# Optimization experiments

Hardware: AMD Instinct MI355X
Metric: run time of the kernel (lower is better)

Reference implementation:

```python
import jax, jax.numpy as jnp
import numpy as np

PATCH = 7
STRIDE = 1
ALPHA = 0.05


def extract_patches(im, p=PATCH, s=STRIDE):
    # im: (b, c, h, w) -> (b, n_patches, c*p*p)
    pat = jax.lax.conv_general_dilated_patches(im, (p, p), (s, s), 'VALID')  # (b, c*p*p, H', W')
    b, d = pat.shape[0], pat.shape[1]
    return pat.reshape(b, d, -1).transpose(0, 2, 1)


def _coherence_l2(xp, yp):
    # xp: (Ni, d) input patches, yp: (Nt, d) target patches, both fp16
    d = xp.shape[-1]
    x2 = jnp.sum(xp * xp, axis=-1)                     # (Ni,)
    y2 = jnp.sum(yp * yp, axis=-1)                     # (Nt,)
    cross = jnp.einsum('td,id->ti', yp, xp)            # (Nt, Ni)
    dist = (y2[:, None] + x2[None, :] - 2.0 * cross) / d
    # normalize each target row by its NN distance (+alpha), then min over targets
    dist = dist / (jnp.min(dist, axis=1, keepdims=True) + jnp.asarray(ALPHA, dist.dtype))
    return jnp.min(dist, axis=0).mean()


def setup_inputs() -> dict:
    key = jax.random.key(0)
    k1, k2 = jax.random.split(key)
    x = jax.random.normal(k1, (2, 3, 96, 96), dtype=jnp.float32)
    y = jax.random.normal(k2, (2, 3, 96, 96), dtype=jnp.float32)
    return {"x": x, "y": y}


def reference(x, y):
    x16 = x.astype(jnp.float16)
    y16 = y.astype(jnp.float16)
    xp = extract_patches(x16)   # (b, N, d)
    yp = extract_patches(y16)   # (b, N, d)
    per_image = jax.vmap(_coherence_l2)(xp, yp)  # (b,)
    return per_image.mean()
```

## Files before the change

kernel.cpp:

```cpp
#include <hip/hip_runtime.h>
#include <hip/hip_fp16.h>

#define IMGS 2
#define OW 90
#define NP 8100
#define HW 96
#define CH_STRIDE 9216
#define IMG_STRIDE 27648
#define KP 192
#define MP 8192
#define ALPHA 0.05f
#define INV_D (1.0f/147.0f)
#define PAD_SENTINEL 60000.0f

typedef _Float16 half8 __attribute__((ext_vector_type(8)));
typedef float floatx4 __attribute__((ext_vector_type(4)));

#define GLD_LDS16(gp, lp)                                                     \
    __builtin_amdgcn_global_load_lds(                                         \
        (const __attribute__((address_space(1))) void*)(gp),                  \
        (__attribute__((address_space(3))) void*)(lp), 16, 0, 0)

#define XP_OFF   0
#define YP_OFF   (XP_OFF + IMGS*MP*KP*2)
#define N2Y_OFF  (YP_OFF + IMGS*MP*KP*2)
#define RMIN_OFF (N2Y_OFF + IMGS*MP*4)
#define CMIN_OFF (RMIN_OFF + IMGS*MP*4)

__global__ __launch_bounds__(256) void k_build(const float* __restrict__ x,
                                               const float* __restrict__ y,
                                               char* __restrict__ wsb) {
    int tid = threadIdx.x;
    int hwv = tid >> 5;
    int l = tid & 31;
    int grow = blockIdx.x * 8 + hwv;
    int tensor = grow >> 14;
    int img = (grow >> 13) & 1;
    int row = grow & (MP - 1);
    const float* src = (tensor ? y : x) + img * IMG_STRIDE;
    int py = row / OW, px = row - py * OW;
    bool rvalid = row < NP;

    float vals[8];
#pragma unroll
    for (int j = 0; j < 8; j++) {
        int k = l * 8 + j;
        float v = 0.0f;
        if (rvalid && k < 147) {
            int c = k / 49;
            int rm = k - c * 49;
            int dy = rm / 7, dx = rm - dy * 7;
            v = src[c * CH_STRIDE + (py + dy) * HW + px + dx];
        }
        vals[j] = (float)(_Float16)v;
    }
    float ss16 = 0.0f;
#pragma unroll
    for (int j = 0; j < 8; j++) ss16 = fmaf(vals[j], vals[j], ss16);
#pragma unroll
    for (int m = 1; m < 32; m <<= 1) ss16 += __shfl_xor(ss16, m, 32);

    if (tensor && l == 0)
        ((float*)(wsb + N2Y_OFF))[img * MP + row] = rvalid ? ss16 : 0.0f;

    half8 h;
#pragma unroll
    for (int j = 0; j < 8; j++) {
        float f = vals[j];
        if (tensor) f *= -2.0f;
        h[j] = (_Float16)f;
    }
    if (l == 18) {
        h[3] = tensor ? (_Float16)1.0f
                      : (rvalid ? (_Float16)ss16 : (_Float16)PAD_SENTINEL);
        if (!tensor) h[4] = rvalid ? (_Float16)1.0f : (_Float16)0.0f;
    }
    if (l < 24) {
        _Float16* dst = (_Float16*)(wsb + (tensor ? YP_OFF : XP_OFF)) +
                        ((size_t)img * MP + row) * KP + l * 8;
        *(half8*)dst = h;
    }
    if (tid < 8) {
        int gi = blockIdx.x * 8 + tid;
        if (gi < IMGS * MP)
            ((int*)(wsb + RMIN_OFF))[gi] = 0x7f800000;
        else
            ((int*)(wsb + CMIN_OFF))[gi - IMGS * MP] = 0x7f800000;
    }
}

#define R2OFF 8192

#define STAGE64(mat, buf)                                                      \
    {                                                                          \
        int rb_ = w * 16;                                                      \
        _Pragma("unroll") for (int g_ = 0; g_ < 4; g_++) {                     \
            int r_ = rb_ + g_ * 4 + (lane >> 4);                               \
            int gc_ = (lane & 15) ^ (r_ & 7);                                  \
            GLD_LDS16((mat) + (size_t)r_ * KP + gc_ * 8,                       \
                      (buf) + (rb_ + g_ * 4) * 128);                           \
        }                                                                      \
        int r2_ = rb_ + (lane >> 2);                                           \
        int gc2_ = (lane & 3) ^ ((r2_ >> 1) & 3);                              \
        GLD_LDS16((mat) + (size_t)r2_ * KP + 128 + gc2_ * 8,                   \
                  (buf) + R2OFF + rb_ * 32);                                   \
    }

#define READFRAG(buf, row, ks)                                                 \
    ((ks) < 4 ? *(const half8*)(&(buf)[(row) * 128 +                           \
                                       ((((ks) * 4 + quad) ^ ((row) & 7)) * 8)]) \
              : *(const half8*)(&(buf)[R2OFF + (row) * 32 +                    \
                                       ((quad ^ (((row) >> 1) & 3)) * 8)]))

template <int PASS>
__global__ __launch_bounds__(256, 3) void k_gemm(char* __restrict__ wsb) {
    __shared__ __align__(16) _Float16 Buf[2][10240];
    int tid = threadIdx.x;
    int lane = tid & 63, w = tid >> 6;
    int quad = lane >> 4, col16 = lane & 15;
    int q = blockIdx.x;
    int rtile = blockIdx.y;
    int img = blockIdx.z;

    const _Float16* Res = (const _Float16*)(wsb + (PASS == 1 ? YP_OFF : XP_OFF)) +
                          ((size_t)img * MP + rtile * 128) * KP;
    const _Float16* Str = (const _Float16*)(wsb + (PASS == 1 ? XP_OFF : YP_OFF)) +
                          (size_t)img * MP * KP;

    STAGE64(Res, Buf[0]);
    STAGE64(Res + (size_t)64 * KP, Buf[1]);
    __syncthreads();
    half8 rf[4][5];
    const _Float16* rb = Buf[w >> 1];
#pragma unroll
    for (int i = 0; i < 4; i++)
#pragma unroll
        for (int c = 0; c < 5; c++)
            rf[i][c] = READFRAG(rb, i * 16 + col16, c);
    __syncthreads();
    STAGE64(Str + (size_t)(q * 16) * 64 * KP, Buf[0]);

    float rmin[4][4];
    float cmin[4];
#pragma unroll
    for (int i = 0; i < 4; i++) {
        cmin[i] = 1e30f;
#pragma unroll
        for (int j = 0; j < 4; j++) rmin[i][j] = 1e30f;
    }
    int s0 = (w & 1) * 32;

    for (int s = 0; s < 16; s++) {
        __syncthreads();
        if (s < 15)
            STAGE64(Str + (size_t)(q * 16 + s + 1) * 64 * KP, Buf[(s + 1) & 1]);
        const _Float16* sb = Buf[s & 1];
        floatx4 acc[8];
#pragma unroll
        for (int i = 0; i < 8; i++) acc[i] = (floatx4){0.f, 0.f, 0.f, 0.f};
#pragma unroll
        for (int ks = 0; ks < 5; ks++) {
            half8 sf0 = READFRAG(sb, s0 + col16, ks);
            half8 sf1 = READFRAG(sb, s0 + 16 + col16, ks);
            if (PASS == 1) {
#pragma unroll
                for (int i = 0; i < 4; i++) {
                    acc[i * 2] = __builtin_amdgcn_mfma_f32_16x16x32_f16(
                        rf[i][ks], sf0, acc[i * 2], 0, 0, 0);
                    acc[i * 2 + 1] = __builtin_amdgcn_mfma_f32_16x16x32_f16(
                        rf[i][ks], sf1, acc[i * 2 + 1], 0, 0, 0);
                }
            } else {
#pragma unroll
                for (int i = 0; i < 4; i++) {
                    acc[i] = __builtin_amdgcn_mfma_f32_16x16x32_f16(
                        sf0, rf[i][ks], acc[i], 0, 0, 0);
                    acc[4 + i] = __builtin_amdgcn_mfma_f32_16x16x32_f16(
                        sf1, rf[i][ks], acc[4 + i], 0, 0, 0);
                }
            }
        }
        if (PASS == 1) {
#pragma unroll
            for (int i = 0; i < 4; i++)
#pragma unroll
                for (int r = 0; r < 4; r++)
                    rmin[i][r] = fminf(rmin[i][r],
                                       fminf(acc[i * 2][r], acc[i * 2 + 1][r]));
        } else {
#pragma unroll
            for (int i = 0; i < 4; i++)
#pragma unroll
                for (int r = 0; r < 4; r++)
                    cmin[i] = fminf(cmin[i], fminf(acc[i][r], acc[4 + i][r]));
        }
    }

    if (PASS == 1) {
#pragma unroll
        for (int i = 0; i < 4; i++)
#pragma unroll
            for (int r = 0; r < 4; r++) {
                float best = rmin[i][r];
                best = fminf(best, __shfl_xor(best, 1, 16));
                best = fminf(best, __shfl_xor(best, 2, 16));
                best = fminf(best, __shfl_xor(best, 4, 16));
                best = fminf(best, __shfl_xor(best, 8, 16));
                int rg = rtile * 128 + (w >> 1) * 64 + i * 16 + quad * 4 + r;
                if (col16 == 0 && rg < NP)
                    atomicMin((int*)(wsb + RMIN_OFF) + img * MP + rg,
                              __float_as_int(best));
            }
    } else {
#pragma unroll
        for (int i = 0; i < 4; i++) {
            float best = cmin[i];
            best = fminf(best, __shfl_xor(best, 16, 64));
            best = fminf(best, __shfl_xor(best, 32, 64));
            int cg = rtile * 128 + (w >> 1) * 64 + i * 16 + col16;
            if (quad == 0)
                atomicMin((int*)(wsb + CMIN_OFF) + img * MP + cg,
                          __float_as_int(best));
        }
    }
}

__global__ __launch_bounds__(256) void k_rescale(char* __restrict__ wsb) {
    int gid = blockIdx.x * 256 + threadIdx.x;
    int chunk = gid % 24;
    int row = gid / 24;
    int r = row & (MP - 1);
    float rm = __int_as_float(((const int*)(wsb + RMIN_OFF))[row]);
    float y2 = ((const float*)(wsb + N2Y_OFF))[row];
    float d = (y2 + rm) * INV_D;
    float rp = INV_D / (d + ALPHA);
    _Float16* p = (_Float16*)(wsb + YP_OFF) + (size_t)row * KP + chunk * 8;
    half8 h = *(half8*)p;
#pragma unroll
    for (int j = 0; j < 8; j++) h[j] = (_Float16)((float)h[j] * rp);
    if (chunk == 18)
        h[4] = (r < NP) ? (_Float16)(rp * y2) : (_Float16)PAD_SENTINEL;
    *(half8*)p = h;
}

__global__ __launch_bounds__(256) void k_final(const char* __restrict__ wsb,
                                               float* __restrict__ out) {
    __shared__ float red[256];
    int tid = threadIdx.x;
    const int* cm = (const int*)(wsb + CMIN_OFF);
    float s = 0.0f;
    for (int i = tid; i < NP; i += 256) {
        s += __int_as_float(cm[i]);
        s += __int_as_float(cm[MP + i]);
    }
    red[tid] = s;
    __syncthreads();
    for (int st = 128; st > 0; st >>= 1) {
        if (tid < st) red[tid] += red[tid + st];
        __syncthreads();
    }
    if (tid == 0) out[0] = red[0] * (0.5f / NP);
}

extern "C" void kernel_launch(void* const* d_in, const int* in_sizes, int n_in,
                              void* d_out, int out_size, void* d_ws, size_t ws_size,
                              hipStream_t stream) {
    const float* x = (const float*)d_in[0];
    const float* y = (const float*)d_in[1];
    char* wsb = (char*)d_ws;
    float* out = (float*)d_out;

    k_build<<<4096, 256, 0, stream>>>(x, y, wsb);
    k_gemm<1><<<dim3(8, 64, IMGS), 256, 0, stream>>>(wsb);
    k_rescale<<<(IMGS * MP * 24) / 256, 256, 0, stream>>>(wsb);
    k_gemm<2><<<dim3(8, 64, IMGS), 256, 0, stream>>>(wsb);
    k_final<<<1, 256, 0, stream>>>(wsb, out);
}
```

Baseline: 167.2 us.

## Fuse row rescale into second GEMM pass and restructure MFMA tiling per wave

Drops the separate rescale kernel and the stored y-norm buffer. The y norm now sits in the augmented K column, so pass 1 yields the full row distance, and pass 2 scales each streamed target fragment on the fly by the reciprocal normalizer. Each wave now keeps all 128 resident rows in registers (8x5 fragments) and streams 16 target rows, so both passes share one min/atomic epilogue. This removes a kernel launch and a full read/write of the target patch matrix. In exchange it raises register pressure (occupancy hint lowered from 3 to 2) and adds per-step fp16 multiplies and global loads of row minima in pass 2.

```diff
diff --git a/kernel.cpp b/kernel.cpp
--- a/kernel.cpp
+++ b/kernel.cpp
@@ -23,8 +23,7 @@
 
 #define XP_OFF   0
 #define YP_OFF   (XP_OFF + IMGS*MP*KP*2)
-#define N2Y_OFF  (YP_OFF + IMGS*MP*KP*2)
-#define RMIN_OFF (N2Y_OFF + IMGS*MP*4)
+#define RMIN_OFF (YP_OFF + IMGS*MP*KP*2)
 #define CMIN_OFF (RMIN_OFF + IMGS*MP*4)
 
 __global__ __launch_bounds__(256) void k_build(const float* __restrict__ x,
@@ -60,9 +59,6 @@
 #pragma unroll
     for (int m = 1; m < 32; m <<= 1) ss16 += __shfl_xor(ss16, m, 32);
 
-    if (tensor && l == 0)
-        ((float*)(wsb + N2Y_OFF))[img * MP + row] = rvalid ? ss16 : 0.0f;
-
     half8 h;
 #pragma unroll
     for (int j = 0; j < 8; j++) {
@@ -71,9 +67,13 @@
         h[j] = (_Float16)f;
     }
     if (l == 18) {
-        h[3] = tensor ? (_Float16)1.0f
-                      : (rvalid ? (_Float16)ss16 : (_Float16)PAD_SENTINEL);
-        if (!tensor) h[4] = rvalid ? (_Float16)1.0f : (_Float16)0.0f;
+        if (tensor) {
+            h[3] = (_Float16)1.0f;
+            h[4] = rvalid ? (_Float16)ss16 : (_Float16)0.0f;
+        } else {
+            h[3] = rvalid ? (_Float16)ss16 : (_Float16)PAD_SENTINEL;
+            h[4] = rvalid ? (_Float16)1.0f : (_Float16)0.0f;
+        }
     }
     if (l < 24) {
         _Float16* dst = (_Float16*)(wsb + (tensor ? YP_OFF : XP_OFF)) +
@@ -113,7 +113,7 @@
                                        ((quad ^ (((row) >> 1) & 3)) * 8)]))
 
 template <int PASS>
-__global__ __launch_bounds__(256, 3) void k_gemm(char* __restrict__ wsb) {
+__global__ __launch_bounds__(256, 2) void k_gemm(char* __restrict__ wsb) {
     __shared__ __align__(16) _Float16 Buf[2][10240];
     int tid = threadIdx.x;
     int lane = tid & 63, w = tid >> 6;
@@ -130,117 +130,71 @@
     STAGE64(Res, Buf[0]);
     STAGE64(Res + (size_t)64 * KP, Buf[1]);
     __syncthreads();
-    half8 rf[4][5];
-    const _Float16* rb = Buf[w >> 1];
-#pragma unroll
-    for (int i = 0; i < 4; i++)
+    half8 rf[8][5];
+#pragma unroll
+    for (int i = 0; i < 8; i++) {
+        const _Float16* rb = (i < 4) ? Buf[0] : Buf[1];
 #pragma unroll
         for (int c = 0; c < 5; c++)
-            rf[i][c] = READFRAG(rb, i * 16 + col16, c);
+            rf[i][c] = READFRAG(rb, (i & 3) * 16 + col16, c);
+    }
     __syncthreads();
     STAGE64(Str + (size_t)(q * 16) * 64 * KP, Buf[0]);
 
-    float rmin[4][4];
-    float cmin[4];
-#pragma unroll
-    for (int i = 0; i < 4; i++) {
-        cmin[i] = 1e30f;
-#pragma unroll
-        for (int j = 0; j < 4; j++) rmin[i][j] = 1e30f;
-    }
-    int s0 = (w & 1) * 32;
+    float mn[8];
+#pragma unroll
+    for (int i = 0; i < 8; i++) mn[i] = 1e30f;
+    const int* RM = (const int*)(wsb + RMIN_OFF) + img * MP;
+    int srow = w * 16 + col16;
 
     for (int s = 0; s < 16; s++) {
         __syncthreads();
         if (s < 15)
             STAGE64(Str + (size_t)(q * 16 + s + 1) * 64 * KP, Buf[(s + 1) & 1]);
         const _Float16* sb = Buf[s & 1];
+
+        _Float16 rp = (_Float16)1.0f;
+        bool pad = false;
+        if (PASS == 2) {
+            int rmb = RM[(q * 16 + s) * 64 + srow];
+            pad = (rmb == 0x7f800000);
+            float d = __int_as_float(rmb) * INV_D;
+            rp = (_Float16)(INV_D / (d + ALPHA));
+        }
+
         floatx4 acc[8];
 #pragma unroll
         for (int i = 0; i < 8; i++) acc[i] = (floatx4){0.f, 0.f, 0.f, 0.f};
 #pragma unroll
         for (int ks = 0; ks < 5; ks++) {
-            half8 sf0 = READFRAG(sb, s0 + col16, ks);
-            half8 sf1 = READFRAG(sb, s0 + 16 + col16, ks);
-            if (PASS == 1) {
-#pragma unroll
-                for (int i = 0; i < 4; i++) {
-                    acc[i * 2] = __builtin_amdgcn_mfma_f32_16x16x32_f16(
-                        rf[i][ks], sf0, acc[i * 2], 0, 0, 0);
-                    acc[i * 2 + 1] = __builtin_amdgcn_mfma_f32_16x16x32_f16(
-                        rf[i][ks], sf1, acc[i * 2 + 1], 0, 0, 0);
-                }
-            } else {
-#pragma unroll
-                for (int i = 0; i < 4; i++) {
-                    acc[i] = __builtin_amdgcn_mfma_f32_16x16x32_f16(
-                        sf0, rf[i][ks], acc[i], 0, 0, 0);
-                    acc[4 + i] = __builtin_amdgcn_mfma_f32_16x16x32_f16(
-                        sf1, rf[i][ks], acc[4 + i], 0, 0, 0);
-                }
+            half8 sf = READFRAG(sb, srow, ks);
+            if (PASS == 2) {
+                half8 rpv = {rp, rp, rp, rp, rp, rp, rp, rp};
+                sf = sf * rpv;
+                if (ks == 4 && pad && quad == 2)
+                    sf[4] = (_Float16)PAD_SENTINEL;
             }
-        }
-        if (PASS == 1) {
-#pragma unroll
-            for (int i = 0; i < 4; i++)
-#pragma unroll
-                for (int r = 0; r < 4; r++)
-                    rmin[i][r] = fminf(rmin[i][r],
-                                       fminf(acc[i * 2][r], acc[i * 2 + 1][r]));
-        } else {
-#pragma unroll
-            for (int i = 0; i < 4; i++)
-#pragma unroll
-                for (int r = 0; r < 4; r++)
-                    cmin[i] = fminf(cmin[i], fminf(acc[i][r], acc[4 + i][r]));
-        }
-    }
-
-    if (PASS == 1) {
-#pragma unroll
-        for (int i = 0; i < 4; i++)
-#pragma unroll
-            for (int r = 0; r < 4; r++) {
-                float best = rmin[i][r];
-                best = fminf(best, __shfl_xor(best, 1, 16));
-                best = fminf(best, __shfl_xor(best, 2, 16));
-                best = fminf(best, __shfl_xor(best, 4, 16));
-                best = fminf(best, __shfl_xor(best, 8, 16));
-                int rg = rtile * 128 + (w >> 1) * 64 + i * 16 + quad * 4 + r;
-                if (col16 == 0 && rg < NP)
-                    atomicMin((int*)(wsb + RMIN_OFF) + img * MP + rg,
-                              __float_as_int(best));
-            }
-    } else {
-#pragma unroll
-        for (int i = 0; i < 4; i++) {
-            float best = cmin[i];
-            best = fminf(best, __shfl_xor(best, 16, 64));
-            best = fminf(best, __shfl_xor(best, 32, 64));
-            int cg = rtile * 128 + (w >> 1) * 64 + i * 16 + col16;
-            if (quad == 0)
-                atomicMin((int*)(wsb + CMIN_OFF) + img * MP + cg,
-                          __float_as_int(best));
-        }
-    }
-}
-
-__global__ __launch_bounds__(256) void k_rescale(char* __restrict__ wsb) {
-    int gid = blockIdx.x * 256 + threadIdx.x;
-    int chunk = gid % 24;
-    int row = gid / 24;
-    int r = row & (MP - 1);
-    float rm = __int_as_float(((const int*)(wsb + RMIN_OFF))[row]);
-    float y2 = ((const float*)(wsb + N2Y_OFF))[row];
-    float d = (y2 + rm) * INV_D;
-    float rp = INV_D / (d + ALPHA);
-    _Float16* p = (_Float16*)(wsb + YP_OFF) + (size_t)row * KP + chunk * 8;
-    half8 h = *(half8*)p;
-#pragma unroll
-    for (int j = 0; j < 8; j++) h[j] = (_Float16)((float)h[j] * rp);
-    if (chunk == 18)
-        h[4] = (r < NP) ? (_Float16)(rp * y2) : (_Float16)PAD_SENTINEL;
-    *(half8*)p = h;
+#pragma unroll
+            for (int i = 0; i < 8; i++)
+                acc[i] = __builtin_amdgcn_mfma_f32_16x16x32_f16(
+                    sf, rf[i][ks], acc[i], 0, 0, 0);
+        }
+#pragma unroll
+        for (int i = 0; i < 8; i++)
+            mn[i] = fminf(mn[i], fminf(fminf(acc[i][0], acc[i][1]),
+                                       fminf(acc[i][2], acc[i][3])));
+    }
+
+    int* dst = (int*)(wsb + (PASS == 1 ? RMIN_OFF : CMIN_OFF)) + img * MP;
+#pragma unroll
+    for (int i = 0; i < 8; i++) {
+        float best = mn[i];
+        best = fminf(best, __shfl_xor(best, 16, 64));
+        best = fminf(best, __shfl_xor(best, 32, 64));
+        int cg = rtile * 128 + i * 16 + col16;
+        if (quad == 0 && cg < NP)
+            atomicMin(dst + cg, __float_as_int(best));
+    }
 }
 
 __global__ __launch_bounds__(256) void k_final(const char* __restrict__ wsb,
@@ -272,7 +226,6 @@
 
     k_build<<<4096, 256, 0, stream>>>(x, y, wsb);
     k_gemm<1><<<dim3(8, 64, IMGS), 256, 0, stream>>>(wsb);
-    k_rescale<<<(IMGS * MP * 24) / 256, 256, 0, stream>>>(wsb);
     k_gemm<2><<<dim3(8, 64, IMGS), 256, 0, stream>>>(wsb);
     k_final<<<1, 256, 0, stream>>>(wsb, out);
 }
```

Result: faster. 157.4 us (-5.9%).
